# Optimization experiments

Measured on AMD Instinct MI355X. Metric: run time of the kernel, lower is better.

## Reference

```python
import jax, jax.numpy as jnp
import numpy as np

B, H, W = 64, 128, 128
K_SIS, K_RANGE = 0.5, 0.3
PSI_SCALE = 0.05
SKIP_W = 0.1
ALPHA_MAX = 0.5
SIGMA, KSIZE = 1.0, 5
DN = ('NCHW', 'OIHW', 'NCHW')


def conv2d(x, w, b, pad):
    y = jax.lax.conv_general_dilated(x, w, (1, 1), [(pad, pad), (pad, pad)], dimension_numbers=DN)
    return y + b[None, :, None, None]


def group_norm(x, groups, gamma, beta, eps=1e-5):
    Bc, C, Hc, Wc = x.shape
    xr = x.reshape(Bc, groups, C // groups, Hc, Wc)
    mu = xr.mean(axis=(2, 3, 4), keepdims=True)
    var = xr.var(axis=(2, 3, 4), keepdims=True)
    xn = ((xr - mu) / jnp.sqrt(var + eps)).reshape(Bc, C, Hc, Wc)
    return xn * gamma[None, :, None, None] + beta[None, :, None, None]


def coords():
    xs = jnp.linspace(-1.0, 1.0, W)
    ys = jnp.linspace(-1.0, 1.0, H)
    X, Y = jnp.meshgrid(xs, ys, indexing='xy')  # (H, W)
    r = jnp.sqrt(X * X + Y * Y)
    phi = jnp.arctan2(Y, X)
    polar = jnp.stack([r, jnp.cos(phi), jnp.sin(phi)], axis=0)  # (3,H,W)
    base_grid = jnp.stack([X, Y], axis=-1)  # (H,W,2)
    return polar, r, base_grid


def gaussian_blur(x):
    off = jnp.arange(KSIZE, dtype=jnp.float32) - (KSIZE - 1) / 2.0
    k1 = jnp.exp(-off * off / (2.0 * SIGMA * SIGMA))
    k1 = k1 / k1.sum()
    p = KSIZE // 2
    xp = jnp.pad(x, ((0, 0), (0, 0), (p, p), (p, p)), mode='reflect')
    xh = jax.lax.conv_general_dilated(xp, k1.reshape(1, 1, 1, KSIZE), (1, 1), [(0, 0), (0, 0)], dimension_numbers=DN)
    return jax.lax.conv_general_dilated(xh, k1.reshape(1, 1, KSIZE, 1), (1, 1), [(0, 0), (0, 0)], dimension_numbers=DN)


def grad_x(a, dx):  # along W (last axis), np.gradient style
    left = a[..., 1:2] - a[..., 0:1]
    mid = (a[..., 2:] - a[..., :-2]) * 0.5
    right = a[..., -1:] - a[..., -2:-1]
    return jnp.concatenate([left, mid, right], axis=-1) / dx


def grad_y(a, dy):  # along H
    top = a[..., 1:2, :] - a[..., 0:1, :]
    mid = (a[..., 2:, :] - a[..., :-2, :]) * 0.5
    bot = a[..., -1:, :] - a[..., -2:-1, :]
    return jnp.concatenate([top, mid, bot], axis=-2) / dy


def soft_clamp(a):
    return ALPHA_MAX * jnp.tanh(a / ALPHA_MAX)


def grid_sample_bilinear_border(img, grid):
    # img (B,1,H,W), grid (B,H,W,2) in [-1,1], align_corners=True, border pad
    Bc, _, Hc, Wc = img.shape
    px = (grid[..., 0] + 1.0) * 0.5 * (Wc - 1)
    py = (grid[..., 1] + 1.0) * 0.5 * (Hc - 1)
    x0 = jnp.floor(px)
    y0 = jnp.floor(py)
    wx = px - x0
    wy = py - y0
    x0i = jnp.clip(x0.astype(jnp.int32), 0, Wc - 1)
    x1i = jnp.clip(x0i + 1, 0, Wc - 1)
    y0i = jnp.clip(y0.astype(jnp.int32), 0, Hc - 1)
    y1i = jnp.clip(y0i + 1, 0, Hc - 1)
    im = img[:, 0]
    bidx = jnp.arange(Bc)[:, None, None]
    g = lambda yy, xx: im[bidx, yy, xx]
    out = (g(y0i, x0i) * (1 - wx) * (1 - wy) + g(y0i, x1i) * wx * (1 - wy)
           + g(y1i, x0i) * (1 - wx) * wy + g(y1i, x1i) * wx * wy)
    return out[:, None, :, :]


def _conv_init(key, shape, scale=None):
    fan_in = shape[1] * shape[2] * shape[3]
    s = scale if scale is not None else 1.0 / np.sqrt(fan_in)
    return jax.random.normal(key, shape, dtype=jnp.float32) * s


def setup_inputs() -> dict:
    key = jax.random.key(0)
    ks = jax.random.split(key, 16)
    d = {'image': jax.random.uniform(ks[0], (B, 1, H, W), dtype=jnp.float32)}
    # KPredictor params
    d['kw1'] = _conv_init(ks[1], (32, 4, 3, 3)); d['kb1'] = jnp.zeros((32,), jnp.float32)
    d['kg1'] = jnp.ones((32,), jnp.float32); d['kbeta1'] = jnp.zeros((32,), jnp.float32)
    d['kw2'] = _conv_init(ks[2], (32, 32, 3, 3)); d['kb2'] = jnp.zeros((32,), jnp.float32)
    d['kg2'] = jnp.ones((32,), jnp.float32); d['kbeta2'] = jnp.zeros((32,), jnp.float32)
    d['kw3'] = _conv_init(ks[3], (16, 32, 3, 3)); d['kb3'] = jnp.zeros((16,), jnp.float32)
    d['kg3'] = jnp.ones((16,), jnp.float32); d['kbeta3'] = jnp.zeros((16,), jnp.float32)
    d['kw4'] = _conv_init(ks[4], (1, 16, 1, 1), scale=0.02); d['kb4'] = jnp.zeros((1,), jnp.float32)
    # PsiResidualPredictor params
    d['pw1'] = _conv_init(ks[5], (16, 4, 3, 3)); d['pb1'] = jnp.zeros((16,), jnp.float32)
    d['pg1'] = jnp.ones((16,), jnp.float32); d['pbeta1'] = jnp.zeros((16,), jnp.float32)
    d['pw2'] = _conv_init(ks[6], (16, 16, 3, 3)); d['pb2'] = jnp.zeros((16,), jnp.float32)
    d['pg2'] = jnp.ones((16,), jnp.float32); d['pbeta2'] = jnp.zeros((16,), jnp.float32)
    d['pw3'] = _conv_init(ks[7], (1, 16, 1, 1), scale=0.02); d['pb3'] = jnp.zeros((1,), jnp.float32)
    return d


def _forward(image, kw1, kb1, kg1, kbeta1, kw2, kb2, kg2, kbeta2, kw3, kb3, kg3, kbeta3,
             kw4, kb4, pw1, pb1, pg1, pbeta1, pw2, pb2, pg2, pbeta2, pw3, pb3):
    polar, theta_abs, base_grid = coords()
    x = jnp.concatenate([image, jnp.broadcast_to(polar[None], (image.shape[0], 3, H, W))], axis=1)
    silu = jax.nn.silu
    # k predictor
    h = silu(group_norm(conv2d(x, kw1, kb1, 1), 8, kg1, kbeta1))
    h = silu(group_norm(conv2d(h, kw2, kb2, 1), 8, kg2, kbeta2))
    h = silu(group_norm(conv2d(h, kw3, kb3, 1), 4, kg3, kbeta3))
    k = K_SIS * (1.0 + K_RANGE * jnp.tanh(conv2d(h, kw4, kb4, 0)))
    # psi residual predictor
    p = silu(group_norm(conv2d(x, pw1, pb1, 1), 4, pg1, pbeta1))
    p = silu(group_norm(conv2d(p, pw2, pb2, 1), 4, pg2, pbeta2))
    psi_res = PSI_SCALE * jnp.tanh(conv2d(p, pw3, pb3, 0))
    psi = k * theta_abs[None, None] + psi_res
    psi_s = gaussian_blur(psi)
    dx = 2.0 / (W - 1)
    dy = 2.0 / (H - 1)
    alpha_x = soft_clamp(grad_x(psi_s, dx))
    alpha_y = soft_clamp(grad_y(psi_s, dy))
    alpha_grid = jnp.stack([alpha_x[:, 0], alpha_y[:, 0]], axis=-1)  # (B,H,W,2)
    beta_grid = jnp.clip(base_grid[None] - alpha_grid, -1.0, 1.0)
    warped = grid_sample_bilinear_border(image, beta_grid)
    source = (1.0 - SKIP_W) * warped + SKIP_W * image
    return source, k, psi, alpha_x, alpha_y


def reference(image, kw1, kb1, kg1, kbeta1, kw2, kb2, kg2, kbeta2, kw3, kb3, kg3, kbeta3,
              kw4, kb4, pw1, pb1, pg1, pbeta1, pw2, pb2, pg2, pbeta2, pw3, pb3):
    return _forward(image, kw1, kb1, kg1, kbeta1, kw2, kb2, kg2, kbeta2, kw3, kb3, kg3,
                    kbeta3, kw4, kb4, pw1, pb1, pg1, pbeta1, pw2, pb2, pg2, pbeta2, pw3, pb3)
```

## Files before the change

### kernel.cpp

```cpp
#include <hip/hip_runtime.h>

static constexpr int H = 128, W = 128, HW = H * W;

typedef __attribute__((ext_vector_type(8))) short short8;
typedef __attribute__((ext_vector_type(4))) float f32x4;
typedef unsigned int uint;
typedef unsigned short ushort;

__device__ __forceinline__ float rcp_f(float x) { return __builtin_amdgcn_rcpf(x); }
__device__ __forceinline__ float silu_f(float v) { return v * rcp_f(1.f + __expf(-v)); }
__device__ __forceinline__ float tanh_f(float x) { return 1.f - 2.f * rcp_f(__expf(2.f * x) + 1.f); }
__device__ __forceinline__ ushort f2bf(float f) {
    uint u = __builtin_bit_cast(uint, f);
    return (ushort)((u + 0x7FFFu + ((u >> 16) & 1u)) >> 16);
}
__device__ __forceinline__ float bf2f(ushort s) {
    return __builtin_bit_cast(float, (uint)s << 16);
}

struct PrepArgs {
    const float *w1, *w2, *w3, *wp1, *wp2;
    float *wt48, *polar, *stats;
    ushort *wpk2h, *wpk2l, *wpk3h, *wpk3l, *wpkph, *wpkpl;
    int nstats;
};

__global__ void prep_k(PrepArgs a) {
    int tid = blockIdx.x * 256 + threadIdx.x;
    int stride = gridDim.x * 256;
    for (int i = tid; i < a.nstats; i += stride) a.stats[i] = 0.f;
    for (int i = tid; i < HW; i += stride) {
        int yy = i >> 7, xx = i & 127;
        float X = -1.f + 2.f * xx / 127.f;
        float Y = -1.f + 2.f * yy / 127.f;
        float r = sqrtf(X * X + Y * Y);
        float inv = (r > 0.f) ? 1.f / r : 0.f;
        a.polar[i] = r;
        a.polar[HW + i] = (r > 0.f) ? X * inv : 1.f;
        a.polar[2 * HW + i] = Y * inv;
    }
    for (int i = tid; i < 36 * 48; i += stride) {
        int t = i / 48, c = i % 48;
        int cin = t / 9, k = t % 9;
        float w = (c < 32) ? a.w1[((c * 4 + cin) * 3 + k / 3) * 3 + k % 3]
                           : a.wp1[(((c - 32) * 4 + cin) * 3 + k / 3) * 3 + k % 3];
        a.wt48[i] = w;
    }
    for (int i = tid; i < 9 * 2 * 64 * 8; i += stride) {
        int j = i & 7, l = (i >> 3) & 63, t = i >> 9;
        int q = t >> 1, nt = t & 1;
        int k = (l >> 4) * 8 + j;
        int n = nt * 16 + (l & 15);
        int ky = q / 3, kx = q % 3;
        float w = a.w2[((n * 32 + k) * 3 + ky) * 3 + kx];
        ushort h = f2bf(w);
        a.wpk2h[i] = h;
        a.wpk2l[i] = f2bf(w - bf2f(h));
    }
    for (int i = tid; i < 9 * 64 * 8; i += stride) {
        int j = i & 7, l = (i >> 3) & 63, q = i >> 9;
        int k = (l >> 4) * 8 + j;
        int n = l & 15;
        int ky = q / 3, kx = q % 3;
        float w = a.w3[((n * 32 + k) * 3 + ky) * 3 + kx];
        ushort h = f2bf(w);
        a.wpk3h[i] = h;
        a.wpk3l[i] = f2bf(w - bf2f(h));
    }
    for (int i = tid; i < 9 * 64 * 8; i += stride) {
        int j = i & 7, l = (i >> 3) & 63, q = i >> 9;
        int k = (l >> 4) * 8 + j;
        int cin = k & 15;
        int n = l & 15;
        float w = a.wp2[((n * 16 + cin) * 3 + q / 3) * 3 + q % 3];
        ushort h = f2bf(w);
        a.wpkph[i] = h;
        a.wpkpl[i] = f2bf(w - bf2f(h));
    }
}

__global__ __launch_bounds__(256) void conv1f_k(
    const float* __restrict__ img, const float* __restrict__ polar,
    const float* __restrict__ wt48,
    const float* __restrict__ kb1, const float* __restrict__ pb1,
    float* __restrict__ outK, float* __restrict__ outP,
    float* __restrict__ st1, float* __restrict__ stp1) {
    const int tid = threadIdx.x;
    const int y = blockIdx.x * 2 + (tid >> 7);
    const int x = tid & 127;
    const int b = blockIdx.y;

    float acc[48];
#pragma unroll
    for (int c = 0; c < 32; c++) acc[c] = kb1[c];
#pragma unroll
    for (int c = 0; c < 16; c++) acc[32 + c] = pb1[c];

#pragma unroll
    for (int cin = 0; cin < 4; cin++) {
        const float* pl = (cin == 0) ? img + (size_t)b * HW : polar + (size_t)(cin - 1) * HW;
#pragma unroll
        for (int ky = 0; ky < 3; ky++) {
            int yy = y + ky - 1;
            if (yy >= 0 && yy < H) {
                const float* row = pl + yy * W;
                float v1 = row[x];
                float v0 = (x > 0) ? row[x - 1] : 0.f;
                float v2 = (x < 127) ? row[x + 1] : 0.f;
                const float* wr = wt48 + (cin * 9 + ky * 3) * 48;
#pragma unroll
                for (int c = 0; c < 48; c++) {
                    acc[c] = fmaf(wr[c], v0, acc[c]);
                    acc[c] = fmaf(wr[48 + c], v1, acc[c]);
                    acc[c] = fmaf(wr[96 + c], v2, acc[c]);
                }
            }
        }
    }

    float4* obK = (float4*)(outK + ((size_t)b * HW + y * W + x) * 32);
#pragma unroll
    for (int i = 0; i < 8; i++)
        obK[i] = make_float4(acc[4 * i], acc[4 * i + 1], acc[4 * i + 2], acc[4 * i + 3]);
    float4* obP = (float4*)(outP + ((size_t)b * HW + y * W + x) * 16);
#pragma unroll
    for (int i = 0; i < 4; i++)
        obP[i] = make_float4(acc[32 + 4 * i], acc[33 + 4 * i], acc[34 + 4 * i], acc[35 + 4 * i]);

    __shared__ float sred[4][12][2];
    const int lane = tid & 63, wid = tid >> 6;
#pragma unroll
    for (int g = 0; g < 12; g++) {
        float s = 0.f, s2 = 0.f;
#pragma unroll
        for (int c = g * 4; c < g * 4 + 4; c++) { s += acc[c]; s2 += acc[c] * acc[c]; }
#pragma unroll
        for (int off = 32; off > 0; off >>= 1) {
            s += __shfl_down(s, off);
            s2 += __shfl_down(s2, off);
        }
        if (lane == 0) { sred[wid][g][0] = s; sred[wid][g][1] = s2; }
    }
    __syncthreads();
    if (tid < 12) {
        float s = 0.f, s2 = 0.f;
#pragma unroll
        for (int w = 0; w < 4; w++) { s += sred[w][tid][0]; s2 += sred[w][tid][1]; }
        float* dst = (tid < 8) ? &st1[((size_t)b * 8 + tid) * 2]
                               : &stp1[((size_t)b * 4 + (tid - 8)) * 2];
        atomicAdd(dst, s);
        atomicAdd(dst + 1, s2);
    }
}

template <int CIN, int COUT, int Gin, int Gout>
__global__ __launch_bounds__(256, 3) void conv_roll_k(
    const float* __restrict__ raw_in, const float* __restrict__ stats_in,
    const float* __restrict__ gamma, const float* __restrict__ beta,
    const float* __restrict__ bias,
    const short8* __restrict__ wph, const short8* __restrict__ wpl,
    float* __restrict__ outraw, float* __restrict__ stats_out) {

    constexpr int LDSC = 2 * CIN;
    constexpr int SWZM = LDSC / 8 - 1;
    constexpr int NCH8 = CIN / 8;
    constexpr int WN = (COUT == 32) ? 2 : 1;
    constexpr int F = (WN == 2) ? 4 : 2;
    constexpr int ROWS = 8;
    constexpr int ROWB = 128 * LDSC * 2;
    constexpr int CHUNKS = 128 * NCH8 / 256;

    __shared__ __align__(16) ushort ring[3 * 128 * LDSC];
    __shared__ float la[CIN], lc[CIN];

    const int tid = threadIdx.x;
    const int wid = tid >> 6, l = tid & 63;
    const int lm = l & 15, lk = l >> 4;
    const int y0 = blockIdx.x * ROWS;
    const int b = blockIdx.y;
    const int wn = (WN == 2) ? (wid & 1) : 0;
    const int pxb = (WN == 2) ? ((wid >> 1) * 64) : (wid * 32);
    const int ch = wn * 16 + lm;

    if (tid < CIN) {
        constexpr float inv = 1.f / ((CIN / Gin) * (float)HW);
        int g = tid / (CIN / Gin);
        float s = stats_in[((size_t)b * Gin + g) * 2];
        float s2 = stats_in[((size_t)b * Gin + g) * 2 + 1];
        float m = s * inv;
        float rs = rsqrtf(s2 * inv - m * m + 1e-5f);
        float aa = gamma[tid] * rs;
        la[tid] = aa;
        lc[tid] = beta[tid] - m * aa;
    }
    __syncthreads();

    short8 wh[9], wl[9];
#pragma unroll
    for (int q = 0; q < 9; q++) {
        wh[q] = wph[(q * WN + wn) * 64 + l];
        wl[q] = wpl[(q * WN + wn) * 64 + l];
    }
    const float bv = bias[ch];
    const short8 Z8 = {0, 0, 0, 0, 0, 0, 0, 0};
    char* tbw = (char*)ring;

    auto load_row = [&](int ys, float4* g0, float4* g1) {
#pragma unroll
        for (int ck = 0; ck < CHUNKS; ck++) {
            int c = tid + ck * 256;
            int px = c / NCH8, ch8 = c % NCH8;
            const float4* gp = (const float4*)(raw_in + (((size_t)b * HW + ys * W + px) * CIN + ch8 * 8));
            g0[ck] = gp[0];
            g1[ck] = gp[1];
        }
    };
    auto stage_row = [&](int ys, int slot, const float4* g0, const float4* g1) {
#pragma unroll
        for (int ck = 0; ck < CHUNKS; ck++) {
            int c = tid + ck * 256;
            int px = c / NCH8, ch8 = c % NCH8;
            short8 hi8, lo8;
            if (ys >= 0 && ys < H) {
                float vv[8] = {g0[ck].x, g0[ck].y, g0[ck].z, g0[ck].w,
                               g1[ck].x, g1[ck].y, g1[ck].z, g1[ck].w};
#pragma unroll
                for (int e = 0; e < 8; e++) {
                    int cc = ch8 * 8 + e;
                    float f = silu_f(fmaf(vv[e], la[cc], lc[cc]));
                    ushort hb = f2bf(f);
                    hi8[e] = (short)hb;
                    lo8[e] = (short)f2bf(f - bf2f(hb));
                }
            } else {
#pragma unroll
                for (int e = 0; e < 8; e++) { hi8[e] = 0; lo8[e] = 0; }
            }
            int inner = px * LDSC * 2 + ch8 * 16;
            int swz = (px & SWZM) << 4;
            char* sb = tbw + slot * ROWB;
            *(short8*)(sb + (inner ^ swz)) = hi8;
            *(short8*)(sb + ((inner + CIN * 2) ^ swz)) = lo8;
        }
    };

    {
        float4 p0[CHUNKS], p1[CHUNKS];
        for (int pr = 0; pr < 3; pr++) {
            int ys = y0 - 1 + pr;
            if (ys >= 0 && ys < H) load_row(ys, p0, p1);
            stage_row(ys, (ys + 3) % 3, p0, p1);
        }
    }
    __syncthreads();

    float sa = 0.f, sa2 = 0.f;
    float4 g0[CHUNKS], g1[CHUNKS];

    for (int r = 0; r < ROWS; r++) {
        const int y = y0 + r;
        const int ys = y + 2;
        const bool do_stage = (r < ROWS - 1);
        if (do_stage && ys < H) load_row(ys, g0, g1);

        f32x4 acc[F];
#pragma unroll
        for (int f = 0; f < F; f++) acc[f] = (f32x4){0.f, 0.f, 0.f, 0.f};

        const char* sbase[3] = {tbw + ((y + 2) % 3) * ROWB,
                                tbw + ((y + 3) % 3) * ROWB,
                                tbw + ((y + 4) % 3) * ROWB};
#pragma unroll
        for (int q = 0; q < 9; q++) {
            const int ky = q / 3, kx = q % 3;
            const char* sb = sbase[ky];
#pragma unroll
            for (int f = 0; f < F; f++) {
                int xb = pxb + f * 16 + lm + kx - 1;
                bool valid = (xb >= 0) && (xb < 128);
                int xbc = min(max(xb, 0), 127);
                int inner = xbc * LDSC * 2;
                int swz = (xbc & SWZM) << 4;
                if constexpr (CIN == 32) {
                    short8 ah = *(const short8*)(sb + ((inner + lk * 16) ^ swz));
                    short8 al = *(const short8*)(sb + ((inner + (lk + 4) * 16) ^ swz));
                    if (!valid) { ah = Z8; al = Z8; }
                    acc[f] = __builtin_amdgcn_mfma_f32_16x16x32_bf16(ah, wh[q], acc[f], 0, 0, 0);
                    acc[f] = __builtin_amdgcn_mfma_f32_16x16x32_bf16(al, wh[q], acc[f], 0, 0, 0);
                    acc[f] = __builtin_amdgcn_mfma_f32_16x16x32_bf16(ah, wl[q], acc[f], 0, 0, 0);
                } else {
                    short8 a = *(const short8*)(sb + ((inner + lk * 16) ^ swz));
                    if (!valid) a = Z8;
                    acc[f] = __builtin_amdgcn_mfma_f32_16x16x32_bf16(a, wh[q], acc[f], 0, 0, 0);
                    acc[f] = __builtin_amdgcn_mfma_f32_16x16x32_bf16(a, wl[q], acc[f], 0, 0, 0);
                }
            }
        }

#pragma unroll
        for (int f = 0; f < F; f++) {
#pragma unroll
            for (int rr = 0; rr < 4; rr++) {
                int x = pxb + f * 16 + lk * 4 + rr;
                float v = acc[f][rr] + bv;
                outraw[((size_t)b * HW + y * W + x) * COUT + ch] = v;
                sa += v;
                sa2 += v * v;
            }
        }
        __syncthreads();
        if (do_stage) stage_row(ys, (ys + 3) % 3, g0, g1);
        __syncthreads();
    }

    float s = sa, s2 = sa2;
    s += __shfl_xor(s, 16); s2 += __shfl_xor(s2, 16);
    s += __shfl_xor(s, 32); s2 += __shfl_xor(s2, 32);
    constexpr int CgO = COUT / Gout;
#pragma unroll
    for (int m = 1; m < CgO; m <<= 1) { s += __shfl_xor(s, m); s2 += __shfl_xor(s2, m); }
    if (l < 16 && (lm & (CgO - 1)) == 0) {
        int g = ch / CgO;
        atomicAdd(&stats_out[((size_t)b * Gout + g) * 2], s);
        atomicAdd(&stats_out[((size_t)b * Gout + g) * 2 + 1], s2);
    }
}

static __device__ __constant__ float GW0 = 0.40261994689423467f;
static __device__ __constant__ float GW1 = 0.24420134200323348f;
static __device__ __constant__ float GW2 = 0.05448868454964433f;

__global__ __launch_bounds__(512) void tail_k(
    const float* __restrict__ h3, const float* __restrict__ p2,
    const float* __restrict__ img,
    const float* __restrict__ kg3, const float* __restrict__ kbeta3,
    const float* __restrict__ st3,
    const float* __restrict__ pg2, const float* __restrict__ pbeta2,
    const float* __restrict__ stp2,
    const float* __restrict__ kw4, const float* __restrict__ kb4,
    const float* __restrict__ pw3, const float* __restrict__ pb3,
    float* __restrict__ osrc, float* __restrict__ outk,
    float* __restrict__ outpsi, float* __restrict__ oax,
    float* __restrict__ oay) {
    __shared__ float psiA[22 * 128];
    __shared__ float psiB[22 * 128];

    const int tid = threadIdx.x;
    const int y0 = blockIdx.x * 16;
    const int b = blockIdx.y;

    constexpr float inv = 1.f / (float)(4 * HW);
    float a3[4], c3[4], ap[4], cp[4];
#pragma unroll
    for (int g = 0; g < 4; g++) {
        float s = st3[((size_t)b * 4 + g) * 2];
        float s2 = st3[((size_t)b * 4 + g) * 2 + 1];
        float m = s * inv;
        a3[g] = rsqrtf(s2 * inv - m * m + 1e-5f);
        c3[g] = m;
        s = stp2[((size_t)b * 4 + g) * 2];
        s2 = stp2[((size_t)b * 4 + g) * 2 + 1];
        m = s * inv;
        ap[g] = rsqrtf(s2 * inv - m * m + 1e-5f);
        cp[g] = m;
    }

    for (int idx = tid; idx < 22 * 128; idx += 512) {
        int s = idx >> 7, j = idx & 127;
        int g = y0 - 3 + s;
        g = (g < 0) ? -g : (g > 127 ? 254 - g : g);
        int rem = g * W + j;

        float hv[16], pv[16];
        const float4* hp = (const float4*)(h3 + ((size_t)b * HW + rem) * 16);
        const float4* pp = (const float4*)(p2 + ((size_t)b * HW + rem) * 16);
#pragma unroll
        for (int t = 0; t < 4; t++) {
            float4 u = hp[t];
            hv[4 * t] = u.x; hv[4 * t + 1] = u.y; hv[4 * t + 2] = u.z; hv[4 * t + 3] = u.w;
            float4 w = pp[t];
            pv[4 * t] = w.x; pv[4 * t + 1] = w.y; pv[4 * t + 2] = w.z; pv[4 * t + 3] = w.w;
        }
        float dk = kb4[0], dp = pb3[0];
#pragma unroll
        for (int c = 0; c < 16; c++) {
            int gg = c >> 2;
            float a = kg3[c] * a3[gg];
            float t = fmaf(hv[c] - c3[gg], a, kbeta3[c]);
            dk = fmaf(kw4[c], silu_f(t), dk);
            a = pg2[c] * ap[gg];
            t = fmaf(pv[c] - cp[gg], a, pbeta2[c]);
            dp = fmaf(pw3[c], silu_f(t), dp);
        }
        float k = 0.5f * (1.f + 0.3f * tanh_f(dk));
        float psr = 0.05f * tanh_f(dp);
        float X = -1.f + 2.f * j / 127.f;
        float Y = -1.f + 2.f * g / 127.f;
        float r = sqrtf(X * X + Y * Y);
        float psi = fmaf(k, r, psr);
        psiA[idx] = psi;
        if (s >= 3 && s < 19) {
            int n = (size_t)b * HW + rem;
            outk[n] = k;
            outpsi[n] = psi;
        }
    }
    __syncthreads();

    for (int idx = tid; idx < 22 * 128; idx += 512) {
        int s = idx >> 7, j = idx & 127;
        const float* row = psiA + s * 128;
        int jm2 = j - 2; jm2 = jm2 < 0 ? -jm2 : jm2;
        int jm1 = j - 1; jm1 = jm1 < 0 ? -jm1 : jm1;
        int jp1 = j + 1; jp1 = jp1 > 127 ? 254 - jp1 : jp1;
        int jp2 = j + 2; jp2 = jp2 > 127 ? 254 - jp2 : jp2;
        psiB[idx] = GW2 * (row[jm2] + row[jp2]) + GW1 * (row[jm1] + row[jp1]) + GW0 * row[j];
    }
    __syncthreads();

    for (int idx = tid; idx < 18 * 128; idx += 512) {
        int s = (idx >> 7) + 2, j = idx & 127;
        psiA[s * 128 + j] = GW2 * (psiB[(s - 2) * 128 + j] + psiB[(s + 2) * 128 + j]) +
                            GW1 * (psiB[(s - 1) * 128 + j] + psiB[(s + 1) * 128 + j]) +
                            GW0 * psiB[s * 128 + j];
    }
    __syncthreads();

    const float* im = img + (size_t)b * HW;
    for (int idx = tid; idx < 16 * 128; idx += 512) {
        int r = idx >> 7, j = idx & 127;
        int y = y0 + r, s = r + 3;
        const float* ps = psiA + s * 128;

        float gx;
        if (j == 0)        gx = ps[1] - ps[0];
        else if (j == 127) gx = ps[127] - ps[126];
        else               gx = (ps[j + 1] - ps[j - 1]) * 0.5f;
        gx *= 63.5f;

        float gy;
        if (y == 0)        gy = psiA[(s + 1) * 128 + j] - ps[j];
        else if (y == 127) gy = ps[j] - psiA[(s - 1) * 128 + j];
        else               gy = (psiA[(s + 1) * 128 + j] - psiA[(s - 1) * 128 + j]) * 0.5f;
        gy *= 63.5f;

        float ax = 0.5f * tanh_f(gx * 2.f);
        float ay = 0.5f * tanh_f(gy * 2.f);

        float X = -1.f + 2.f * j / 127.f;
        float Y = -1.f + 2.f * y / 127.f;
        float bx = fminf(fmaxf(X - ax, -1.f), 1.f);
        float by = fminf(fmaxf(Y - ay, -1.f), 1.f);
        float px = (bx + 1.f) * 0.5f * 127.f;
        float py = (by + 1.f) * 0.5f * 127.f;
        float x0f = floorf(px), y0f = floorf(py);
        float wx = px - x0f, wy = py - y0f;
        int x0i = min(max((int)x0f, 0), 127);
        int x1i = min(x0i + 1, 127);
        int y0i = min(max((int)y0f, 0), 127);
        int y1i = min(y0i + 1, 127);

        float v00 = im[y0i * W + x0i], v01 = im[y0i * W + x1i];
        float v10 = im[y1i * W + x0i], v11 = im[y1i * W + x1i];
        float wrp = v00 * (1.f - wx) * (1.f - wy) + v01 * wx * (1.f - wy) +
                    v10 * (1.f - wx) * wy + v11 * wx * wy;

        int n = (size_t)b * HW + y * W + j;
        osrc[n] = 0.9f * wrp + 0.1f * im[y * W + j];
        oax[n] = ax;
        oay[n] = ay;
    }
}

extern "C" void kernel_launch(void* const* d_in, const int* in_sizes, int n_in,
                              void* d_out, int out_size, void* d_ws, size_t ws_size,
                              hipStream_t stream) {
    const float* img = (const float*)d_in[0];
    const int B = in_sizes[0] / HW;
    const int npix = B * HW;

    char* base = (char*)d_ws;
    size_t off = 0;
    auto alloc = [&](size_t bytes) {
        char* p = base + off;
        off = (off + bytes + 255) & ~(size_t)255;
        return p;
    };

    float* polar = (float*)alloc(3 * HW * 4);
    float* wt48  = (float*)alloc(36 * 48 * 4);
    ushort* wpk2h = (ushort*)alloc(9 * 2 * 64 * 8 * 2);
    ushort* wpk2l = (ushort*)alloc(9 * 2 * 64 * 8 * 2);
    ushort* wpk3h = (ushort*)alloc(9 * 64 * 8 * 2);
    ushort* wpk3l = (ushort*)alloc(9 * 64 * 8 * 2);
    ushort* wpkph = (ushort*)alloc(9 * 64 * 8 * 2);
    ushort* wpkpl = (ushort*)alloc(9 * 64 * 8 * 2);
    int nstats = B * 56;
    float* stats = (float*)alloc((size_t)nstats * 4);
    float* st1  = stats;
    float* st2  = st1 + (size_t)B * 16;
    float* st3  = st2 + (size_t)B * 16;
    float* stp1 = st3 + (size_t)B * 8;
    float* stp2 = stp1 + (size_t)B * 8;
    size_t head = off;

    int BC = B;
    while (BC > 1) {
        size_t need = head + (size_t)BC * HW * 80 * 4 + 3 * 256;
        if (need <= ws_size) break;
        BC >>= 1;
    }
    float* R   = (float*)alloc((size_t)BC * HW * 32 * 4);
    float* R2  = (float*)alloc((size_t)BC * HW * 32 * 4);
    float* p2B = (float*)alloc((size_t)BC * HW * 16 * 4);
    float* RpB = R2;
    float* h3B = R;

    float* outsrc = (float*)d_out;
    float* outk   = outsrc + (size_t)npix;
    float* outpsi = outk + (size_t)npix;
    float* outax  = outpsi + (size_t)npix;
    float* outay  = outax + (size_t)npix;

    PrepArgs pa;
    pa.w1 = (const float*)d_in[1]; pa.w2 = (const float*)d_in[5];
    pa.w3 = (const float*)d_in[9]; pa.wp1 = (const float*)d_in[15];
    pa.wp2 = (const float*)d_in[19];
    pa.wt48 = wt48; pa.polar = polar; pa.stats = stats;
    pa.wpk2h = wpk2h; pa.wpk2l = wpk2l; pa.wpk3h = wpk3h; pa.wpk3l = wpk3l;
    pa.wpkph = wpkph; pa.wpkpl = wpkpl; pa.nstats = nstats;
    prep_k<<<128, 256, 0, stream>>>(pa);

    for (int b0 = 0; b0 < B; b0 += BC) {
        const float* imgc = img + (size_t)b0 * HW;
        dim3 cgf(H / 2, BC), cgr(H / 8, BC);

        conv1f_k<<<cgf, 256, 0, stream>>>(imgc, polar, wt48,
                                          (const float*)d_in[2], (const float*)d_in[16],
                                          R, RpB, st1 + (size_t)b0 * 16, stp1 + (size_t)b0 * 8);

        conv_roll_k<16, 16, 4, 4><<<cgr, 256, 0, stream>>>(
            RpB, stp1 + (size_t)b0 * 8, (const float*)d_in[17], (const float*)d_in[18],
            (const float*)d_in[20], (const short8*)wpkph, (const short8*)wpkpl,
            p2B, stp2 + (size_t)b0 * 8);

        conv_roll_k<32, 32, 8, 8><<<cgr, 256, 0, stream>>>(
            R, st1 + (size_t)b0 * 16, (const float*)d_in[3], (const float*)d_in[4],
            (const float*)d_in[6], (const short8*)wpk2h, (const short8*)wpk2l,
            R2, st2 + (size_t)b0 * 16);
        conv_roll_k<32, 16, 8, 4><<<cgr, 256, 0, stream>>>(
            R2, st2 + (size_t)b0 * 16, (const float*)d_in[7], (const float*)d_in[8],
            (const float*)d_in[10], (const short8*)wpk3h, (const short8*)wpk3l,
            h3B, st3 + (size_t)b0 * 8);

        tail_k<<<dim3(8, BC), 512, 0, stream>>>(
            h3B, p2B, imgc,
            (const float*)d_in[11], (const float*)d_in[12], st3 + (size_t)b0 * 8,
            (const float*)d_in[21], (const float*)d_in[22], stp2 + (size_t)b0 * 8,
            (const float*)d_in[13], (const float*)d_in[14],
            (const float*)d_in[23], (const float*)d_in[24],
            outsrc + (size_t)b0 * HW, outk + (size_t)b0 * HW,
            outpsi + (size_t)b0 * HW, outax + (size_t)b0 * HW,
            outay + (size_t)b0 * HW);
    }
}
```

Baseline: 379.0 us.

## Fuse prep into conv1 head kernel and merge parallel conv2 launches

Removes the separate prep kernel by computing polar coordinates inline in the first conv and packing MFMA weights in extra blocks of the same launch. Stats are zeroed with a memset. The two independent second-stage convs (k-branch and psi-branch) run as one grid via a shared device body. The psi intermediate is staged in the output buffer so it no longer aliases R2, which allows the merge. The aim is fewer launches and better occupancy. The trade-off is extra per-pixel math and unpacked, strided weight reads in conv1.

New measurement: 677.9 us. 78.9% more time.

```diff
diff --git a/kernel.cpp b/kernel.cpp
--- a/kernel.cpp
+++ b/kernel.cpp
@@ -18,111 +18,106 @@
     return __builtin_bit_cast(float, (uint)s << 16);
 }
 
-struct PrepArgs {
-    const float *w1, *w2, *w3, *wp1, *wp2;
-    float *wt48, *polar, *stats;
+struct HeadArgs {
+    const float *img, *w1, *kb1, *wp1, *pb1;
+    const float *w2, *w3, *wp2;
+    float *outK, *outP, *st1, *stp1;
     ushort *wpk2h, *wpk2l, *wpk3h, *wpk3l, *wpkph, *wpkpl;
-    int nstats;
 };
 
-__global__ void prep_k(PrepArgs a) {
-    int tid = blockIdx.x * 256 + threadIdx.x;
-    int stride = gridDim.x * 256;
-    for (int i = tid; i < a.nstats; i += stride) a.stats[i] = 0.f;
-    for (int i = tid; i < HW; i += stride) {
-        int yy = i >> 7, xx = i & 127;
-        float X = -1.f + 2.f * xx / 127.f;
-        float Y = -1.f + 2.f * yy / 127.f;
-        float r = sqrtf(X * X + Y * Y);
-        float inv = (r > 0.f) ? 1.f / r : 0.f;
-        a.polar[i] = r;
-        a.polar[HW + i] = (r > 0.f) ? X * inv : 1.f;
-        a.polar[2 * HW + i] = Y * inv;
-    }
-    for (int i = tid; i < 36 * 48; i += stride) {
-        int t = i / 48, c = i % 48;
-        int cin = t / 9, k = t % 9;
-        float w = (c < 32) ? a.w1[((c * 4 + cin) * 3 + k / 3) * 3 + k % 3]
-                           : a.wp1[(((c - 32) * 4 + cin) * 3 + k / 3) * 3 + k % 3];
-        a.wt48[i] = w;
-    }
-    for (int i = tid; i < 9 * 2 * 64 * 8; i += stride) {
-        int j = i & 7, l = (i >> 3) & 63, t = i >> 9;
-        int q = t >> 1, nt = t & 1;
-        int k = (l >> 4) * 8 + j;
-        int n = nt * 16 + (l & 15);
-        int ky = q / 3, kx = q % 3;
-        float w = a.w2[((n * 32 + k) * 3 + ky) * 3 + kx];
-        ushort h = f2bf(w);
-        a.wpk2h[i] = h;
-        a.wpk2l[i] = f2bf(w - bf2f(h));
-    }
-    for (int i = tid; i < 9 * 64 * 8; i += stride) {
-        int j = i & 7, l = (i >> 3) & 63, q = i >> 9;
-        int k = (l >> 4) * 8 + j;
-        int n = l & 15;
-        int ky = q / 3, kx = q % 3;
-        float w = a.w3[((n * 32 + k) * 3 + ky) * 3 + kx];
-        ushort h = f2bf(w);
-        a.wpk3h[i] = h;
-        a.wpk3l[i] = f2bf(w - bf2f(h));
-    }
-    for (int i = tid; i < 9 * 64 * 8; i += stride) {
-        int j = i & 7, l = (i >> 3) & 63, q = i >> 9;
-        int k = (l >> 4) * 8 + j;
-        int cin = k & 15;
-        int n = l & 15;
-        float w = a.wp2[((n * 16 + cin) * 3 + q / 3) * 3 + q % 3];
-        ushort h = f2bf(w);
-        a.wpkph[i] = h;
-        a.wpkpl[i] = f2bf(w - bf2f(h));
-    }
-}
-
-__global__ __launch_bounds__(256) void conv1f_k(
-    const float* __restrict__ img, const float* __restrict__ polar,
-    const float* __restrict__ wt48,
-    const float* __restrict__ kb1, const float* __restrict__ pb1,
-    float* __restrict__ outK, float* __restrict__ outP,
-    float* __restrict__ st1, float* __restrict__ stp1) {
+__global__ __launch_bounds__(256) void head_k(HeadArgs a) {
     const int tid = threadIdx.x;
+
+    if (blockIdx.x >= 64) {
+        int pb = (blockIdx.x - 64) * gridDim.y + blockIdx.y;
+        int stride = 2 * gridDim.y * 256;
+        int t0 = pb * 256 + tid;
+        for (int i = t0; i < 9 * 2 * 64 * 8; i += stride) {
+            int j = i & 7, l = (i >> 3) & 63, t = i >> 9;
+            int q = t >> 1, nt = t & 1;
+            int k = (l >> 4) * 8 + j;
+            int n = nt * 16 + (l & 15);
+            float w = a.w2[((n * 32 + k) * 3 + q / 3) * 3 + q % 3];
+            ushort h = f2bf(w);
+            a.wpk2h[i] = h;
+            a.wpk2l[i] = f2bf(w - bf2f(h));
+        }
+        for (int i = t0; i < 9 * 64 * 8; i += stride) {
+            int j = i & 7, l = (i >> 3) & 63, q = i >> 9;
+            int k = (l >> 4) * 8 + j;
+            int n = l & 15;
+            float w = a.w3[((n * 32 + k) * 3 + q / 3) * 3 + q % 3];
+            ushort h = f2bf(w);
+            a.wpk3h[i] = h;
+            a.wpk3l[i] = f2bf(w - bf2f(h));
+        }
+        for (int i = t0; i < 9 * 64 * 8; i += stride) {
+            int j = i & 7, l = (i >> 3) & 63, q = i >> 9;
+            int k = (l >> 4) * 8 + j;
+            int cin = k & 15;
+            int n = l & 15;
+            float w = a.wp2[((n * 16 + cin) * 3 + q / 3) * 3 + q % 3];
+            ushort h = f2bf(w);
+            a.wpkph[i] = h;
+            a.wpkpl[i] = f2bf(w - bf2f(h));
+        }
+        return;
+    }
+
     const int y = blockIdx.x * 2 + (tid >> 7);
     const int x = tid & 127;
     const int b = blockIdx.y;
 
     float acc[48];
 #pragma unroll
-    for (int c = 0; c < 32; c++) acc[c] = kb1[c];
-#pragma unroll
-    for (int c = 0; c < 16; c++) acc[32 + c] = pb1[c];
-
-#pragma unroll
-    for (int cin = 0; cin < 4; cin++) {
-        const float* pl = (cin == 0) ? img + (size_t)b * HW : polar + (size_t)(cin - 1) * HW;
-#pragma unroll
-        for (int ky = 0; ky < 3; ky++) {
-            int yy = y + ky - 1;
-            if (yy >= 0 && yy < H) {
-                const float* row = pl + yy * W;
-                float v1 = row[x];
-                float v0 = (x > 0) ? row[x - 1] : 0.f;
-                float v2 = (x < 127) ? row[x + 1] : 0.f;
-                const float* wr = wt48 + (cin * 9 + ky * 3) * 48;
-#pragma unroll
-                for (int c = 0; c < 48; c++) {
-                    acc[c] = fmaf(wr[c], v0, acc[c]);
-                    acc[c] = fmaf(wr[48 + c], v1, acc[c]);
-                    acc[c] = fmaf(wr[96 + c], v2, acc[c]);
+    for (int c = 0; c < 32; c++) acc[c] = a.kb1[c];
+#pragma unroll
+    for (int c = 0; c < 16; c++) acc[32 + c] = a.pb1[c];
+
+#pragma unroll
+    for (int ky = 0; ky < 3; ky++) {
+        int yy = y + ky - 1;
+        if (yy >= 0 && yy < H) {
+            float vals[4][3];
+            const float* row = a.img + (size_t)b * HW + yy * W;
+            vals[0][0] = (x > 0) ? row[x - 1] : 0.f;
+            vals[0][1] = row[x];
+            vals[0][2] = (x < 127) ? row[x + 1] : 0.f;
+            float Yv = -1.f + 2.f * yy / 127.f;
+#pragma unroll
+            for (int dx = 0; dx < 3; dx++) {
+                int xx = x + dx - 1;
+                if (xx < 0 || xx > 127) {
+                    vals[1][dx] = 0.f; vals[2][dx] = 0.f; vals[3][dx] = 0.f;
+                } else {
+                    float Xv = -1.f + 2.f * xx / 127.f;
+                    float r = sqrtf(Xv * Xv + Yv * Yv);
+                    float inv = (r > 0.f) ? rcp_f(r) : 0.f;
+                    vals[1][dx] = r;
+                    vals[2][dx] = (r > 0.f) ? Xv * inv : 1.f;
+                    vals[3][dx] = Yv * inv;
                 }
             }
-        }
-    }
-
-    float4* obK = (float4*)(outK + ((size_t)b * HW + y * W + x) * 32);
+#pragma unroll
+            for (int cin = 0; cin < 4; cin++) {
+                float v0 = vals[cin][0], v1 = vals[cin][1], v2 = vals[cin][2];
+#pragma unroll
+                for (int c = 0; c < 48; c++) {
+                    const float* wb = (c < 32) ? (a.w1 + ((c * 4 + cin) * 3 + ky) * 3)
+                                               : (a.wp1 + (((c - 32) * 4 + cin) * 3 + ky) * 3);
+                    acc[c] = fmaf(wb[0], v0, acc[c]);
+                    acc[c] = fmaf(wb[1], v1, acc[c]);
+                    acc[c] = fmaf(wb[2], v2, acc[c]);
+                }
+            }
+        }
+    }
+
+    float4* obK = (float4*)(a.outK + ((size_t)b * HW + y * W + x) * 32);
 #pragma unroll
     for (int i = 0; i < 8; i++)
         obK[i] = make_float4(acc[4 * i], acc[4 * i + 1], acc[4 * i + 2], acc[4 * i + 3]);
-    float4* obP = (float4*)(outP + ((size_t)b * HW + y * W + x) * 16);
+    float4* obP = (float4*)(a.outP + ((size_t)b * HW + y * W + x) * 16);
 #pragma unroll
     for (int i = 0; i < 4; i++)
         obP[i] = make_float4(acc[32 + 4 * i], acc[33 + 4 * i], acc[34 + 4 * i], acc[35 + 4 * i]);
@@ -146,15 +141,16 @@
         float s = 0.f, s2 = 0.f;
 #pragma unroll
         for (int w = 0; w < 4; w++) { s += sred[w][tid][0]; s2 += sred[w][tid][1]; }
-        float* dst = (tid < 8) ? &st1[((size_t)b * 8 + tid) * 2]
-                               : &stp1[((size_t)b * 4 + (tid - 8)) * 2];
+        float* dst = (tid < 8) ? &a.st1[((size_t)b * 8 + tid) * 2]
+                               : &a.stp1[((size_t)b * 4 + (tid - 8)) * 2];
         atomicAdd(dst, s);
         atomicAdd(dst + 1, s2);
     }
 }
 
 template <int CIN, int COUT, int Gin, int Gout>
-__global__ __launch_bounds__(256, 3) void conv_roll_k(
+__device__ __forceinline__ void conv_roll_body(
+    int bx, int b, ushort* ringp, float* la, float* lc,
     const float* __restrict__ raw_in, const float* __restrict__ stats_in,
     const float* __restrict__ gamma, const float* __restrict__ beta,
     const float* __restrict__ bias,
@@ -170,14 +166,10 @@
     constexpr int ROWB = 128 * LDSC * 2;
     constexpr int CHUNKS = 128 * NCH8 / 256;
 
-    __shared__ __align__(16) ushort ring[3 * 128 * LDSC];
-    __shared__ float la[CIN], lc[CIN];
-
     const int tid = threadIdx.x;
     const int wid = tid >> 6, l = tid & 63;
     const int lm = l & 15, lk = l >> 4;
-    const int y0 = blockIdx.x * ROWS;
-    const int b = blockIdx.y;
+    const int y0 = bx * ROWS;
     const int wn = (WN == 2) ? (wid & 1) : 0;
     const int pxb = (WN == 2) ? ((wid >> 1) * 64) : (wid * 32);
     const int ch = wn * 16 + lm;
@@ -203,7 +195,7 @@
     }
     const float bv = bias[ch];
     const short8 Z8 = {0, 0, 0, 0, 0, 0, 0, 0};
-    char* tbw = (char*)ring;
+    char* tbw = (char*)ringp;
 
     auto load_row = [&](int ys, float4* g0, float4* g1) {
 #pragma unroll
@@ -326,6 +318,41 @@
     }
 }
 
+struct MidArgs {
+    const float *R, *st1, *kg1, *kbeta1, *kb2;
+    const short8 *w2h, *w2l;
+    float *R2, *st2;
+    const float *Rp, *stp1, *pg1, *pbeta1, *pb2;
+    const short8 *wph, *wpl;
+    float *p2, *stp2;
+};
+
+__global__ __launch_bounds__(256, 3) void conv_mid_k(MidArgs a) {
+    __shared__ __align__(16) ushort ring[3 * 128 * 64];
+    __shared__ float la[32], lc[32];
+    if (blockIdx.x < 16)
+        conv_roll_body<32, 32, 8, 8>(blockIdx.x, blockIdx.y, ring, la, lc,
+                                     a.R, a.st1, a.kg1, a.kbeta1, a.kb2,
+                                     a.w2h, a.w2l, a.R2, a.st2);
+    else
+        conv_roll_body<16, 16, 4, 4>(blockIdx.x - 16, blockIdx.y, ring, la, lc,
+                                     a.Rp, a.stp1, a.pg1, a.pbeta1, a.pb2,
+                                     a.wph, a.wpl, a.p2, a.stp2);
+}
+
+__global__ __launch_bounds__(256, 3) void conv3_k(
+    const float* __restrict__ raw_in, const float* __restrict__ stats_in,
+    const float* __restrict__ gamma, const float* __restrict__ beta,
+    const float* __restrict__ bias,
+    const short8* __restrict__ wph, const short8* __restrict__ wpl,
+    float* __restrict__ outraw, float* __restrict__ stats_out) {
+    __shared__ __align__(16) ushort ring[3 * 128 * 64];
+    __shared__ float la[32], lc[32];
+    conv_roll_body<32, 16, 8, 4>(blockIdx.x, blockIdx.y, ring, la, lc,
+                                 raw_in, stats_in, gamma, beta, bias,
+                                 wph, wpl, outraw, stats_out);
+}
+
 static __device__ __constant__ float GW0 = 0.40261994689423467f;
 static __device__ __constant__ float GW1 = 0.24420134200323348f;
 static __device__ __constant__ float GW2 = 0.05448868454964433f;
@@ -487,8 +514,6 @@
         return p;
     };
 
-    float* polar = (float*)alloc(3 * HW * 4);
-    float* wt48  = (float*)alloc(36 * 48 * 4);
     ushort* wpk2h = (ushort*)alloc(9 * 2 * 64 * 8 * 2);
     ushort* wpk2l = (ushort*)alloc(9 * 2 * 64 * 8 * 2);
     ushort* wpk3h = (ushort*)alloc(9 * 64 * 8 * 2);
@@ -502,18 +527,18 @@
     float* st3  = st2 + (size_t)B * 16;
     float* stp1 = st3 + (size_t)B * 8;
     float* stp2 = stp1 + (size_t)B * 8;
-    size_t head = off;
-
+    size_t head_off = off;
+
+    const size_t chb = (size_t)HW * 4;
+    bool rp_out = (head_off + (size_t)B * chb * 80 + 3 * 256 <= ws_size);
     int BC = B;
-    while (BC > 1) {
-        size_t need = head + (size_t)BC * HW * 80 * 4 + 3 * 256;
-        if (need <= ws_size) break;
-        BC >>= 1;
-    }
+    if (!rp_out)
+        while (BC > 1 && head_off + (size_t)BC * chb * 96 + 4 * 256 > ws_size) BC >>= 1;
+
     float* R   = (float*)alloc((size_t)BC * HW * 32 * 4);
     float* R2  = (float*)alloc((size_t)BC * HW * 32 * 4);
     float* p2B = (float*)alloc((size_t)BC * HW * 16 * 4);
-    float* RpB = R2;
+    float* RpB = rp_out ? (float*)d_out : (float*)alloc((size_t)BC * HW * 16 * 4);
     float* h3B = R;
 
     float* outsrc = (float*)d_out;
@@ -522,33 +547,37 @@
     float* outax  = outpsi + (size_t)npix;
     float* outay  = outax + (size_t)npix;
 
-    PrepArgs pa;
-    pa.w1 = (const float*)d_in[1]; pa.w2 = (const float*)d_in[5];
-    pa.w3 = (const float*)d_in[9]; pa.wp1 = (const float*)d_in[15];
-    pa.wp2 = (const float*)d_in[19];
-    pa.wt48 = wt48; pa.polar = polar; pa.stats = stats;
-    pa.wpk2h = wpk2h; pa.wpk2l = wpk2l; pa.wpk3h = wpk3h; pa.wpk3l = wpk3l;
-    pa.wpkph = wpkph; pa.wpkpl = wpkpl; pa.nstats = nstats;
-    prep_k<<<128, 256, 0, stream>>>(pa);
+    hipMemsetAsync(stats, 0, (size_t)nstats * 4, stream);
 
     for (int b0 = 0; b0 < B; b0 += BC) {
         const float* imgc = img + (size_t)b0 * HW;
-        dim3 cgf(H / 2, BC), cgr(H / 8, BC);
-
-        conv1f_k<<<cgf, 256, 0, stream>>>(imgc, polar, wt48,
-                                          (const float*)d_in[2], (const float*)d_in[16],
-                                          R, RpB, st1 + (size_t)b0 * 16, stp1 + (size_t)b0 * 8);
-
-        conv_roll_k<16, 16, 4, 4><<<cgr, 256, 0, stream>>>(
-            RpB, stp1 + (size_t)b0 * 8, (const float*)d_in[17], (const float*)d_in[18],
-            (const float*)d_in[20], (const short8*)wpkph, (const short8*)wpkpl,
-            p2B, stp2 + (size_t)b0 * 8);
-
-        conv_roll_k<32, 32, 8, 8><<<cgr, 256, 0, stream>>>(
-            R, st1 + (size_t)b0 * 16, (const float*)d_in[3], (const float*)d_in[4],
-            (const float*)d_in[6], (const short8*)wpk2h, (const short8*)wpk2l,
-            R2, st2 + (size_t)b0 * 16);
-        conv_roll_k<32, 16, 8, 4><<<cgr, 256, 0, stream>>>(
+
+        HeadArgs ha;
+        ha.img = imgc;
+        ha.w1 = (const float*)d_in[1];  ha.kb1 = (const float*)d_in[2];
+        ha.wp1 = (const float*)d_in[15]; ha.pb1 = (const float*)d_in[16];
+        ha.w2 = (const float*)d_in[5];  ha.w3 = (const float*)d_in[9];
+        ha.wp2 = (const float*)d_in[19];
+        ha.outK = R; ha.outP = RpB;
+        ha.st1 = st1 + (size_t)b0 * 16; ha.stp1 = stp1 + (size_t)b0 * 8;
+        ha.wpk2h = wpk2h; ha.wpk2l = wpk2l; ha.wpk3h = wpk3h; ha.wpk3l = wpk3l;
+        ha.wpkph = wpkph; ha.wpkpl = wpkpl;
+        head_k<<<dim3(66, BC), 256, 0, stream>>>(ha);
+
+        MidArgs ma;
+        ma.R = R; ma.st1 = st1 + (size_t)b0 * 16;
+        ma.kg1 = (const float*)d_in[3]; ma.kbeta1 = (const float*)d_in[4];
+        ma.kb2 = (const float*)d_in[6];
+        ma.w2h = (const short8*)wpk2h; ma.w2l = (const short8*)wpk2l;
+        ma.R2 = R2; ma.st2 = st2 + (size_t)b0 * 16;
+        ma.Rp = RpB; ma.stp1 = stp1 + (size_t)b0 * 8;
+        ma.pg1 = (const float*)d_in[17]; ma.pbeta1 = (const float*)d_in[18];
+        ma.pb2 = (const float*)d_in[20];
+        ma.wph = (const short8*)wpkph; ma.wpl = (const short8*)wpkpl;
+        ma.p2 = p2B; ma.stp2 = stp2 + (size_t)b0 * 8;
+        conv_mid_k<<<dim3(32, BC), 256, 0, stream>>>(ma);
+
+        conv3_k<<<dim3(16, BC), 256, 0, stream>>>(
             R2, st2 + (size_t)b0 * 16, (const float*)d_in[7], (const float*)d_in[8],
             (const float*)d_in[10], (const short8*)wpk3h, (const short8*)wpk3l,
             h3B, st3 + (size_t)b0 * 8);
```
